# Optimization experiments

Measured on AMD Instinct MI355X. Metric: run time of the kernel, lower is better.

## Reference

```python
import jax, jax.numpy as jnp
import numpy as np

BN_EPS = 1e-5

def _batchnorm(x):
    # BatchNorm1d(affine=False) in training mode: per-feature batch stats, biased var
    m = jnp.mean(x, axis=0)
    v = jnp.var(x, axis=0)
    return (x - m) * jax.lax.rsqrt(v + BN_EPS)

def setup_inputs() -> dict:
    key = jax.random.key(0)
    ks = jax.random.split(key, 8)
    B, S, H, I = 2, 2048, 1024, 4096
    NE, NS, K = 16384, 128, 16
    return {
        "hidden_states": jax.random.normal(ks[0], (B, S, H), dtype=jnp.float32),
        "gate_w": jax.random.normal(ks[1], (I, H), dtype=jnp.float32) * 0.02,
        "up_w": jax.random.normal(ks[2], (I, H), dtype=jnp.float32) * 0.02,
        "down_w": jax.random.normal(ks[3], (H, I), dtype=jnp.float32) * 0.02,
        "router_x_w": jax.random.normal(ks[4], (NS, H), dtype=jnp.float32) * 0.02,
        "router_y_w": jax.random.normal(ks[5], (NS, H), dtype=jnp.float32) * 0.02,
        "up_embed": jax.random.normal(ks[6], (NE, H), dtype=jnp.float32) * 0.02,
        "down_embed": jax.random.normal(ks[7], (NE, H), dtype=jnp.float32) * 0.02,
        "top_k": K,
    }

def reference(hidden_states, gate_w, up_w, down_w, router_x_w, router_y_w, up_embed, down_embed, top_k):
    B, S, H = hidden_states.shape
    ns = router_x_w.shape[0]  # num_expert_sqrt
    x = hidden_states.reshape(-1, H)  # [N, H], N = B*S

    # product-key router: two grid log-softmaxes, outer-sum, global top-k
    lpx = jax.nn.log_softmax(_batchnorm(x @ router_x_w.T), axis=-1)  # [N, ns]
    lpy = jax.nn.log_softmax(_batchnorm(x @ router_y_w.T), axis=-1)  # [N, ns]
    all_scores = (lpx[:, :, None] + lpy[:, None, :]).reshape(-1, ns * ns)  # [N, ns^2]
    scores, indices = jax.lax.top_k(all_scores, top_k)  # [N, k]
    routing_weights = jnp.exp(scores)

    # per-token expert embedding gather + small bmm chain (PEER-style)
    ue = up_embed[indices]    # [N, k, H]
    de = down_embed[indices]  # [N, k, H]
    ew = jnp.einsum('nkh,nh->nk', ue, x)
    ew = jax.nn.silu(ew) * routing_weights
    experts_states = jnp.einsum('nk,nkh->nh', ew, de).reshape(B, S, H)

    # dense gated MLP
    dense = (jax.nn.silu(x @ gate_w.T) * (x @ up_w.T)) @ down_w.T
    return dense.reshape(B, S, H) + experts_states
```

## Files before the change

kernel.cpp:

```cpp
#include <hip/hip_runtime.h>

typedef float f32x4 __attribute__((ext_vector_type(4)));
typedef short bf16x8 __attribute__((ext_vector_type(8)));
typedef unsigned short u16;

#define NEG_INF (-1e30f)

__device__ __forceinline__ u16 f2bf(float f) {
    unsigned u = __builtin_bit_cast(unsigned, f);
    unsigned r = u + 0x7FFFu + ((u >> 16) & 1u);
    return (u16)(r >> 16);
}
__device__ __forceinline__ unsigned pk2(float a, float b) {
    unsigned r;
    asm("v_cvt_pk_bf16_f32 %0, %1, %2" : "=v"(r) : "v"(a), "v"(b));
    return r;
}

__device__ __forceinline__ float wave_max(float v) {
    #pragma unroll
    for (int o = 32; o > 0; o >>= 1) v = fmaxf(v, __shfl_xor(v, o, 64));
    return v;
}
__device__ __forceinline__ float wave_sum(float v) {
    #pragma unroll
    for (int o = 32; o > 0; o >>= 1) v += __shfl_xor(v, o, 64);
    return v;
}
__device__ __forceinline__ void wave_argmax(float& v, int& i) {
    #pragma unroll
    for (int o = 32; o > 0; o >>= 1) {
        float ov = __shfl_xor(v, o, 64);
        int oi = __shfl_xor(i, o, 64);
        if (ov > v || (ov == v && oi < i)) { v = ov; i = oi; }
    }
}

__device__ __forceinline__ void g2l16(const void* g, void* l) {
    __builtin_amdgcn_global_load_lds((__attribute__((address_space(1))) void*)g,
                                     (__attribute__((address_space(3))) void*)l,
                                     16, 0, 0);
}
__device__ __forceinline__ int swz8(int row, int c) { return c ^ (row & 7); }
__device__ __forceinline__ int swz4(int row, int c) { return c ^ ((row >> 1) & 3); }

template<int NTHR>
__device__ __forceinline__ void stageA64(const u16* __restrict__ src, int ld,
                                         u16* dst, int tid) {
    #pragma unroll
    for (int r = 0; r < 2; ++r) {
        int e = r * NTHR * 8 + tid * 8;
        int row = e >> 6, c = (e >> 3) & 7;
        g2l16(src + (size_t)row * ld + swz8(row, c) * 8, dst + e);
    }
}
__device__ __forceinline__ void stageA32(const u16* __restrict__ src, int ld,
                                         u16* dst, int tid) {
    #pragma unroll
    for (int r = 0; r < 2; ++r) {
        int e = r * 2048 + tid * 8;
        int row = e >> 5, c = (e >> 3) & 3;
        g2l16(src + (size_t)row * ld + swz4(row, c) * 8, dst + e);
    }
}

__device__ __forceinline__ void loadT64_256(const float* __restrict__ src, int ld,
                                            int tid, float4* v) {
    int row = tid >> 2, col = (tid & 3) * 16;
    const float* s = src + (size_t)row * ld + col;
    v[0] = *reinterpret_cast<const float4*>(s);
    v[1] = *reinterpret_cast<const float4*>(s + 4);
    v[2] = *reinterpret_cast<const float4*>(s + 8);
    v[3] = *reinterpret_cast<const float4*>(s + 12);
}
__device__ __forceinline__ void writeT64_256(const float4* v, u16* dst, int tid) {
    int row = tid >> 2, c0 = (tid & 3) * 2;
    uint4 p0 = { pk2(v[0].x, v[0].y), pk2(v[0].z, v[0].w), pk2(v[1].x, v[1].y), pk2(v[1].z, v[1].w) };
    uint4 p1 = { pk2(v[2].x, v[2].y), pk2(v[2].z, v[2].w), pk2(v[3].x, v[3].y), pk2(v[3].z, v[3].w) };
    *reinterpret_cast<uint4*>(dst + row * 64 + swz8(row, c0) * 8) = p0;
    *reinterpret_cast<uint4*>(dst + row * 64 + swz8(row, c0 + 1) * 8) = p1;
}
__device__ __forceinline__ void loadT64_512(const float* __restrict__ src, int ld,
                                            int tid, float4* v) {
    int row = tid >> 3, col = (tid & 7) * 8;
    const float* s = src + (size_t)row * ld + col;
    v[0] = *reinterpret_cast<const float4*>(s);
    v[1] = *reinterpret_cast<const float4*>(s + 4);
}
__device__ __forceinline__ void writeT64_512(const float4* v, u16* dst, int tid) {
    int row = tid >> 3, c = tid & 7;
    uint4 p = { pk2(v[0].x, v[0].y), pk2(v[0].z, v[0].w), pk2(v[1].x, v[1].y), pk2(v[1].z, v[1].w) };
    *reinterpret_cast<uint4*>(dst + row * 64 + swz8(row, c) * 8) = p;
}
__device__ __forceinline__ void loadT32(const float* __restrict__ src, int ld,
                                        int tid, float4* v) {
    int row = tid >> 1, col = (tid & 1) * 16;
    const float* s = src + (size_t)row * ld + col;
    v[0] = *reinterpret_cast<const float4*>(s);
    v[1] = *reinterpret_cast<const float4*>(s + 4);
    v[2] = *reinterpret_cast<const float4*>(s + 8);
    v[3] = *reinterpret_cast<const float4*>(s + 12);
}
__device__ __forceinline__ void writeT32(const float4* v, u16* dst, int tid) {
    int row = tid >> 1, c0 = (tid & 1) * 2;
    uint4 p0 = { pk2(v[0].x, v[0].y), pk2(v[0].z, v[0].w), pk2(v[1].x, v[1].y), pk2(v[1].z, v[1].w) };
    uint4 p1 = { pk2(v[2].x, v[2].y), pk2(v[2].z, v[2].w), pk2(v[3].x, v[3].y), pk2(v[3].z, v[3].w) };
    *reinterpret_cast<uint4*>(dst + row * 32 + swz4(row, c0) * 8) = p0;
    *reinterpret_cast<uint4*>(dst + row * 32 + swz4(row, c0 + 1) * 8) = p1;
}

__device__ __forceinline__ bf16x8 frag64s(const u16* lds, int row0, int ks, int lane) {
    int row = row0 + (lane & 15);
    int c = ks * 4 + (lane >> 4);
    return *reinterpret_cast<const bf16x8*>(lds + row * 64 + swz8(row, c) * 8);
}
__device__ __forceinline__ bf16x8 frag32s(const u16* lds, int row0, int lane) {
    int row = row0 + (lane & 15);
    int c = lane >> 4;
    return *reinterpret_cast<const bf16x8*>(lds + row * 32 + swz4(row, c) * 8);
}

__global__ void conv_x(const float* __restrict__ s, u16* __restrict__ d) {
    size_t i = (size_t)blockIdx.x * 256 + threadIdx.x;
    float4 v = *reinterpret_cast<const float4*>(s + i * 4);
    uint2 pk;
    pk.x = pk2(v.x, v.y); pk.y = pk2(v.z, v.w);
    *reinterpret_cast<uint2*>(d + i * 4) = pk;
}

template<bool ABF>
__global__ __launch_bounds__(256, 2) void gemm_router(
    const float* __restrict__ Xf, const u16* __restrict__ Xb,
    const float* __restrict__ RX, const float* __restrict__ RY,
    float* __restrict__ R) {
    __shared__ __align__(16) u16 As[2][4096];
    __shared__ __align__(16) u16 Bs[2][4096];
    int tid = threadIdx.x, lane = tid & 63, wave = tid >> 6;
    int rowBase = blockIdx.y * 64, colBase = blockIdx.x * 64;
    const float* Bp = (blockIdx.x < 2) ? RX + (size_t)colBase * 1024
                                       : RY + (size_t)(colBase - 128) * 1024;
    int wm = (wave >> 1) * 32, wn = (wave & 1) * 32;
    f32x4 acc[2][2] = {};
    float4 av[4], bv[4];
    if constexpr (ABF) stageA64<256>(Xb + (size_t)rowBase * 1024, 1024, As[0], tid);
    else               { loadT64_256(Xf + (size_t)rowBase * 1024, 1024, tid, av);
                         writeT64_256(av, As[0], tid); }
    loadT64_256(Bp, 1024, tid, bv);
    writeT64_256(bv, Bs[0], tid);
    __syncthreads();
    int cur = 0;
    for (int t = 0; t < 16; ++t) {
        if (t < 15) {
            int k0 = (t + 1) * 64;
            if constexpr (ABF) stageA64<256>(Xb + (size_t)rowBase * 1024 + k0, 1024, As[cur ^ 1], tid);
            else               loadT64_256(Xf + (size_t)rowBase * 1024 + k0, 1024, tid, av);
            loadT64_256(Bp + k0, 1024, tid, bv);
        }
        #pragma unroll
        for (int ks = 0; ks < 2; ++ks) {
            bf16x8 af[2], bfr[2];
            #pragma unroll
            for (int i = 0; i < 2; ++i) af[i] = frag64s(As[cur], wm + i * 16, ks, lane);
            #pragma unroll
            for (int j = 0; j < 2; ++j) bfr[j] = frag64s(Bs[cur], wn + j * 16, ks, lane);
            #pragma unroll
            for (int i = 0; i < 2; ++i)
                #pragma unroll
                for (int j = 0; j < 2; ++j)
                    acc[i][j] = __builtin_amdgcn_mfma_f32_16x16x32_bf16(af[i], bfr[j], acc[i][j], 0, 0, 0);
        }
        if (t < 15) {
            if constexpr (!ABF) writeT64_256(av, As[cur ^ 1], tid);
            writeT64_256(bv, Bs[cur ^ 1], tid);
        }
        __syncthreads();
        cur ^= 1;
    }
    int rq = (lane >> 4) * 4, cq = lane & 15;
    #pragma unroll
    for (int i = 0; i < 2; ++i)
        #pragma unroll
        for (int j = 0; j < 2; ++j) {
            int col = colBase + wn + j * 16 + cq;
            #pragma unroll
            for (int r = 0; r < 4; ++r) {
                int row = rowBase + wm + i * 16 + rq + r;
                R[(size_t)row * 256 + col] = acc[i][j][r];
            }
        }
}

template<bool ABF>
__global__ __launch_bounds__(256, 2) void gemm_gateup(
    const float* __restrict__ Xf, const u16* __restrict__ Xb,
    const float* __restrict__ GW, const float* __restrict__ UW,
    u16* __restrict__ H2) {
    __shared__ __align__(16) u16 As[2][4096];
    __shared__ __align__(16) u16 Gs[2][4096];
    __shared__ __align__(16) u16 Us[2][4096];
    int tid = threadIdx.x, lane = tid & 63, wave = tid >> 6;
    int b = blockIdx.x, xcd = b & 7, ii = b >> 3;
    int by = xcd * 4 + (ii >> 5), bx = ii & 31;
    int rowBase = by * 128, colBase = bx * 128;
    const float* Gp = GW + (size_t)colBase * 1024;
    const float* Up = UW + (size_t)colBase * 1024;
    int wm = (wave >> 1) * 64, wn = (wave & 1) * 64;
    f32x4 accg[4][4] = {}, accu[4][4] = {};
    float4 av[4], gv[4], uv[4];
    if constexpr (ABF) stageA32(Xb + (size_t)rowBase * 1024, 1024, As[0], tid);
    else               { loadT32(Xf + (size_t)rowBase * 1024, 1024, tid, av);
                         writeT32(av, As[0], tid); }
    loadT32(Gp, 1024, tid, gv);
    loadT32(Up, 1024, tid, uv);
    writeT32(gv, Gs[0], tid);
    writeT32(uv, Us[0], tid);
    __syncthreads();
    int cur = 0;
    for (int t = 0; t < 32; ++t) {
        if (t < 31) {
            int k0 = (t + 1) * 32;
            if constexpr (ABF) stageA32(Xb + (size_t)rowBase * 1024 + k0, 1024, As[cur ^ 1], tid);
            else               loadT32(Xf + (size_t)rowBase * 1024 + k0, 1024, tid, av);
            loadT32(Gp + k0, 1024, tid, gv);
            loadT32(Up + k0, 1024, tid, uv);
        }
        bf16x8 gf[4], uf[4];
        #pragma unroll
        for (int j = 0; j < 4; ++j) { gf[j] = frag32s(Gs[cur], wn + j * 16, lane);
                                      uf[j] = frag32s(Us[cur], wn + j * 16, lane); }
        #pragma unroll
        for (int i = 0; i < 4; ++i) {
            bf16x8 af = frag32s(As[cur], wm + i * 16, lane);
            #pragma unroll
            for (int j = 0; j < 4; ++j) {
                accg[i][j] = __builtin_amdgcn_mfma_f32_16x16x32_bf16(af, gf[j], accg[i][j], 0, 0, 0);
                accu[i][j] = __builtin_amdgcn_mfma_f32_16x16x32_bf16(af, uf[j], accu[i][j], 0, 0, 0);
            }
        }
        if (t < 31) {
            if constexpr (!ABF) writeT32(av, As[cur ^ 1], tid);
            writeT32(gv, Gs[cur ^ 1], tid);
            writeT32(uv, Us[cur ^ 1], tid);
        }
        __syncthreads();
        cur ^= 1;
    }
    int rq = (lane >> 4) * 4, cq = lane & 15;
    #pragma unroll
    for (int i = 0; i < 4; ++i)
        #pragma unroll
        for (int j = 0; j < 4; ++j) {
            int col = colBase + wn + j * 16 + cq;
            #pragma unroll
            for (int r = 0; r < 4; ++r) {
                int row = rowBase + wm + i * 16 + rq + r;
                float gvv = accg[i][j][r], uvv = accu[i][j][r];
                float h = (gvv / (1.f + __expf(-gvv))) * uvv;
                H2[(size_t)row * 4096 + col] = f2bf(h);
            }
        }
}

__global__ __launch_bounds__(512, 4) void gemm_down_pipe(
    const u16* __restrict__ H2, const float* __restrict__ DW, float* __restrict__ Out) {
    __shared__ __align__(16) u16 As[2][8192];
    __shared__ __align__(16) u16 Bs[2][4096];
    int tid = threadIdx.x, lane = tid & 63, wave = tid >> 6;
    int b = blockIdx.x, xcd = b & 7, ii = b >> 3;
    int by = xcd * 4 + (ii >> 4), bx = ii & 15;
    int rowBase = by * 128, colBase = bx * 64;
    const u16* Ap = H2 + (size_t)rowBase * 4096;
    const float* Bp = DW + (size_t)colBase * 4096;
    int wm = (wave >> 1) * 32, wn = (wave & 1) * 32;
    f32x4 acc[2][2] = {};
    float4 bv[2];
    stageA64<512>(Ap, 4096, As[0], tid);
    loadT64_512(Bp, 4096, tid, bv);
    writeT64_512(bv, Bs[0], tid);
    __syncthreads();
    int cur = 0;
    for (int t = 0; t < 64; ++t) {
        if (t < 63) {
            int k0 = (t + 1) * 64;
            stageA64<512>(Ap + k0, 4096, As[cur ^ 1], tid);
            loadT64_512(Bp + k0, 4096, tid, bv);
        }
        #pragma unroll
        for (int ks = 0; ks < 2; ++ks) {
            bf16x8 af[2], bfr[2];
            #pragma unroll
            for (int i = 0; i < 2; ++i) af[i] = frag64s(As[cur], wm + i * 16, ks, lane);
            #pragma unroll
            for (int j = 0; j < 2; ++j) bfr[j] = frag64s(Bs[cur], wn + j * 16, ks, lane);
            #pragma unroll
            for (int i = 0; i < 2; ++i)
                #pragma unroll
                for (int j = 0; j < 2; ++j)
                    acc[i][j] = __builtin_amdgcn_mfma_f32_16x16x32_bf16(af[i], bfr[j], acc[i][j], 0, 0, 0);
        }
        if (t < 63) writeT64_512(bv, Bs[cur ^ 1], tid);
        __syncthreads();
        cur ^= 1;
    }
    int rq = (lane >> 4) * 4, cq = lane & 15;
    #pragma unroll
    for (int i = 0; i < 2; ++i)
        #pragma unroll
        for (int j = 0; j < 2; ++j) {
            int col = colBase + wn + j * 16 + cq;
            #pragma unroll
            for (int r = 0; r < 4; ++r) {
                int row = rowBase + wm + i * 16 + rq + r;
                size_t o = (size_t)row * 1024 + col;
                Out[o] = acc[i][j][r] + Out[o];
            }
        }
}

__global__ __launch_bounds__(256) void expert_store(
    const float* __restrict__ X, const float* __restrict__ UE, const float* __restrict__ DE,
    const int* __restrict__ idxs, const float* __restrict__ wts, float* __restrict__ Out) {
    int n = blockIdx.x, tid = threadIdx.x;
    int lane = tid & 63, wave = tid >> 6;
    __shared__ float xs[1024];
    __shared__ float ews[16];
    __shared__ int sidx[16];
    __shared__ float swt[16];
    if (tid < 16) {
        sidx[tid] = min(max(idxs[n * 16 + tid], 0), 16383);
        swt[tid] = wts[n * 16 + tid];
    }
    {
        float4 v = reinterpret_cast<const float4*>(X + (size_t)n * 1024)[tid];
        *reinterpret_cast<float4*>(xs + tid * 4) = v;
    }
    __syncthreads();
    #pragma unroll
    for (int q = 0; q < 4; ++q) {
        int e = wave * 4 + q;
        const float* row = UE + (size_t)sidx[e] * 1024;
        float acc = 0.f;
        #pragma unroll
        for (int c = 0; c < 4; ++c) {
            int h = c * 256 + lane * 4;
            float4 a = *reinterpret_cast<const float4*>(row + h);
            float4 xv = *reinterpret_cast<const float4*>(xs + h);
            acc += a.x * xv.x + a.y * xv.y + a.z * xv.z + a.w * xv.w;
        }
        acc = wave_sum(acc);
        if (lane == 0) {
            float s = acc / (1.f + __expf(-acc));
            ews[e] = s * swt[e];
        }
    }
    __syncthreads();
    float4 a = make_float4(0.f, 0.f, 0.f, 0.f);
    int h = tid * 4;
    #pragma unroll
    for (int e = 0; e < 16; ++e) {
        const float* row = DE + (size_t)sidx[e] * 1024;
        float4 v = *reinterpret_cast<const float4*>(row + h);
        float w = ews[e];
        a.x += w * v.x; a.y += w * v.y;
        a.z += w * v.z; a.w += w * v.w;
    }
    reinterpret_cast<float4*>(Out + (size_t)n * 1024)[tid] = a;
}

__global__ void bn_stats(const float* __restrict__ R, float* __restrict__ stats) {
    int c = threadIdx.x;
    int r0 = blockIdx.x * 64;
    float s = 0.f, s2 = 0.f;
    for (int r = r0; r < r0 + 64; ++r) {
        float v = R[(size_t)r * 256 + c];
        s += v; s2 += v * v;
    }
    atomicAdd(&stats[c], s);
    atomicAdd(&stats[256 + c], s2);
}

__global__ __launch_bounds__(64) void router_topk(
    const float* __restrict__ R, const float* __restrict__ stats,
    int* __restrict__ idx_out, float* __restrict__ wt_out) {
    int n = blockIdx.x, lane = threadIdx.x;
    const float invN = 1.0f / 4096.0f;
    float z[4];
    #pragma unroll
    for (int p = 0; p < 4; ++p) {
        int c = p * 64 + lane;
        float mean = stats[c] * invN;
        float var = fmaxf(stats[256 + c] * invN - mean * mean, 0.f);
        float v = R[(size_t)n * 256 + c];
        z[p] = (v - mean) * rsqrtf(var + 1e-5f);
    }
    float mx = wave_max(fmaxf(z[0], z[1]));
    float sx = __logf(wave_sum(__expf(z[0] - mx) + __expf(z[1] - mx)));
    float lx0 = z[0] - mx - sx, lx1 = z[1] - mx - sx;
    float my = wave_max(fmaxf(z[2], z[3]));
    float sy = __logf(wave_sum(__expf(z[2] - my) + __expf(z[3] - my)));
    float ly0 = z[2] - my - sy, ly1 = z[3] - my - sy;

    __shared__ float tx[16], ty[16];
    __shared__ int txc[16], tyc[16];
    float v0 = lx0, v1 = lx1;
    for (int t = 0; t < 16; ++t) {
        float bv; int bc;
        if (v1 > v0) { bv = v1; bc = lane + 64; } else { bv = v0; bc = lane; }
        wave_argmax(bv, bc);
        if (lane == 0) { tx[t] = bv; txc[t] = bc; }
        if (bc == lane) v0 = NEG_INF;
        else if (bc == lane + 64) v1 = NEG_INF;
    }
    v0 = ly0; v1 = ly1;
    for (int t = 0; t < 16; ++t) {
        float bv; int bc;
        if (v1 > v0) { bv = v1; bc = lane + 64; } else { bv = v0; bc = lane; }
        wave_argmax(bv, bc);
        if (lane == 0) { ty[t] = bv; tyc[t] = bc; }
        if (bc == lane) v0 = NEG_INF;
        else if (bc == lane + 64) v1 = NEG_INF;
    }
    __syncthreads();
    float cv[4]; int ci[4];
    #pragma unroll
    for (int p = 0; p < 4; ++p) {
        int pid = p * 64 + lane;
        cv[p] = tx[pid >> 4] + ty[pid & 15];
        ci[p] = pid;
    }
    for (int t = 0; t < 16; ++t) {
        float bv = cv[0]; int bc = ci[0];
        #pragma unroll
        for (int p = 1; p < 4; ++p)
            if (cv[p] > bv) { bv = cv[p]; bc = ci[p]; }
        wave_argmax(bv, bc);
        if (lane == 0) {
            idx_out[n * 16 + t] = txc[bc >> 4] * 128 + tyc[bc & 15];
            wt_out[n * 16 + t] = __expf(bv);
        }
        #pragma unroll
        for (int p = 0; p < 4; ++p)
            if (ci[p] == bc) cv[p] = NEG_INF;
    }
}

extern "C" void kernel_launch(void* const* d_in, const int* in_sizes, int n_in,
                              void* d_out, int out_size, void* d_ws, size_t ws_size,
                              hipStream_t stream) {
    const float* x   = (const float*)d_in[0];
    const float* gw  = (const float*)d_in[1];
    const float* uw  = (const float*)d_in[2];
    const float* dw  = (const float*)d_in[3];
    const float* rxw = (const float*)d_in[4];
    const float* ryw = (const float*)d_in[5];
    const float* ue  = (const float*)d_in[6];
    const float* de  = (const float*)d_in[7];
    float* out = (float*)d_out;

    char* p = (char*)d_ws;
    float* stats = (float*)p; p += 16384;
    int*   idxb  = (int*)p;   p += 262144;
    float* wtb   = (float*)p; p += 262144;
    float* R     = (float*)p;
    u16*   H2    = (u16*)p;

    bool useXb = ws_size >= 42483712ull;
    u16* xb = (u16*)((char*)d_ws + 34095104ull);

    hipMemsetAsync(stats, 0, 512 * sizeof(float), stream);
    if (useXb) conv_x<<<4096, 256, 0, stream>>>(x, xb);

    if (useXb) gemm_router<true ><<<dim3(4, 64), 256, 0, stream>>>(x, xb, rxw, ryw, R);
    else       gemm_router<false><<<dim3(4, 64), 256, 0, stream>>>(x, (const u16*)x, rxw, ryw, R);
    bn_stats<<<64, 256, 0, stream>>>(R, stats);
    router_topk<<<4096, 64, 0, stream>>>(R, stats, idxb, wtb);
    expert_store<<<4096, 256, 0, stream>>>(x, ue, de, idxb, wtb, out);

    if (useXb) gemm_gateup<true ><<<1024, 256, 0, stream>>>(x, xb, gw, uw, H2);
    else       gemm_gateup<false><<<1024, 256, 0, stream>>>(x, (const u16*)x, gw, uw, H2);
    gemm_down_pipe<<<512, 512, 0, stream>>>(H2, dw, out);
}
```

Measured before the change: 515.9 us.

## Pre-convert MLP weights to bf16 once per call and retile down GEMM

Adds a conv_all kernel that converts x and the gate, up and down weights to bf16 in workspace, as long as the workspace is large enough. The gate/up and down GEMMs can then stage bf16 tiles directly instead of loading fp32 and packing in-loop. The down GEMM is also reworked from 512-thread 128-row tiles to 256-thread 64-row tiles with more blocks, and gateup's launch bounds are raised to 3 blocks per SM. The cost is an extra conversion pass over roughly 48MB of weights per call, and the new path only runs if ws_size reaches the larger threshold.

Result: slower. 565.8 us (+9.7%).

```diff
diff --git a/kernel.cpp b/kernel.cpp
--- a/kernel.cpp
+++ b/kernel.cpp
@@ -80,18 +80,6 @@
     *reinterpret_cast<uint4*>(dst + row * 64 + swz8(row, c0) * 8) = p0;
     *reinterpret_cast<uint4*>(dst + row * 64 + swz8(row, c0 + 1) * 8) = p1;
 }
-__device__ __forceinline__ void loadT64_512(const float* __restrict__ src, int ld,
-                                            int tid, float4* v) {
-    int row = tid >> 3, col = (tid & 7) * 8;
-    const float* s = src + (size_t)row * ld + col;
-    v[0] = *reinterpret_cast<const float4*>(s);
-    v[1] = *reinterpret_cast<const float4*>(s + 4);
-}
-__device__ __forceinline__ void writeT64_512(const float4* v, u16* dst, int tid) {
-    int row = tid >> 3, c = tid & 7;
-    uint4 p = { pk2(v[0].x, v[0].y), pk2(v[0].z, v[0].w), pk2(v[1].x, v[1].y), pk2(v[1].z, v[1].w) };
-    *reinterpret_cast<uint4*>(dst + row * 64 + swz8(row, c) * 8) = p;
-}
 __device__ __forceinline__ void loadT32(const float* __restrict__ src, int ld,
                                         int tid, float4* v) {
     int row = tid >> 1, col = (tid & 1) * 16;
@@ -126,6 +114,24 @@
     uint2 pk;
     pk.x = pk2(v.x, v.y); pk.y = pk2(v.z, v.w);
     *reinterpret_cast<uint2*>(d + i * 4) = pk;
+}
+__global__ void conv_all(const float* __restrict__ s0, const float* __restrict__ s1,
+                         const float* __restrict__ s2, const float* __restrict__ s3,
+                         u16* __restrict__ d0, u16* __restrict__ d1,
+                         u16* __restrict__ d2, u16* __restrict__ d3) {
+    int b = blockIdx.x, t = threadIdx.x;
+    int seg = b >> 10;
+    const float* s = seg == 0 ? s0 : seg == 1 ? s1 : seg == 2 ? s2 : s3;
+    u16* d = seg == 0 ? d0 : seg == 1 ? d1 : seg == 2 ? d2 : d3;
+    int base = (b & 1023) * 256 + t;
+    #pragma unroll
+    for (int j = 0; j < 4; ++j) {
+        size_t i = (size_t)base + (size_t)j * 262144;
+        float4 v = *reinterpret_cast<const float4*>(s + i * 4);
+        uint2 pk;
+        pk.x = pk2(v.x, v.y); pk.y = pk2(v.z, v.w);
+        *reinterpret_cast<uint2*>(d + i * 4) = pk;
+    }
 }
 
 template<bool ABF>
@@ -190,10 +196,11 @@
         }
 }
 
-template<bool ABF>
-__global__ __launch_bounds__(256, 2) void gemm_gateup(
+template<int MODE>
+__global__ __launch_bounds__(256, 3) void gemm_gateup(
     const float* __restrict__ Xf, const u16* __restrict__ Xb,
-    const float* __restrict__ GW, const float* __restrict__ UW,
+    const float* __restrict__ GWf, const float* __restrict__ UWf,
+    const u16* __restrict__ GWb, const u16* __restrict__ UWb,
     u16* __restrict__ H2) {
     __shared__ __align__(16) u16 As[2][4096];
     __shared__ __align__(16) u16 Gs[2][4096];
@@ -202,27 +209,35 @@
     int b = blockIdx.x, xcd = b & 7, ii = b >> 3;
     int by = xcd * 4 + (ii >> 5), bx = ii & 31;
     int rowBase = by * 128, colBase = bx * 128;
-    const float* Gp = GW + (size_t)colBase * 1024;
-    const float* Up = UW + (size_t)colBase * 1024;
     int wm = (wave >> 1) * 64, wn = (wave & 1) * 64;
     f32x4 accg[4][4] = {}, accu[4][4] = {};
     float4 av[4], gv[4], uv[4];
-    if constexpr (ABF) stageA32(Xb + (size_t)rowBase * 1024, 1024, As[0], tid);
-    else               { loadT32(Xf + (size_t)rowBase * 1024, 1024, tid, av);
-                         writeT32(av, As[0], tid); }
-    loadT32(Gp, 1024, tid, gv);
-    loadT32(Up, 1024, tid, uv);
-    writeT32(gv, Gs[0], tid);
-    writeT32(uv, Us[0], tid);
+    if constexpr (MODE >= 1) stageA32(Xb + (size_t)rowBase * 1024, 1024, As[0], tid);
+    else                     { loadT32(Xf + (size_t)rowBase * 1024, 1024, tid, av);
+                               writeT32(av, As[0], tid); }
+    if constexpr (MODE == 2) {
+        stageA32(GWb + (size_t)colBase * 1024, 1024, Gs[0], tid);
+        stageA32(UWb + (size_t)colBase * 1024, 1024, Us[0], tid);
+    } else {
+        loadT32(GWf + (size_t)colBase * 1024, 1024, tid, gv);
+        loadT32(UWf + (size_t)colBase * 1024, 1024, tid, uv);
+        writeT32(gv, Gs[0], tid);
+        writeT32(uv, Us[0], tid);
+    }
     __syncthreads();
     int cur = 0;
     for (int t = 0; t < 32; ++t) {
         if (t < 31) {
             int k0 = (t + 1) * 32;
-            if constexpr (ABF) stageA32(Xb + (size_t)rowBase * 1024 + k0, 1024, As[cur ^ 1], tid);
-            else               loadT32(Xf + (size_t)rowBase * 1024 + k0, 1024, tid, av);
-            loadT32(Gp + k0, 1024, tid, gv);
-            loadT32(Up + k0, 1024, tid, uv);
+            if constexpr (MODE >= 1) stageA32(Xb + (size_t)rowBase * 1024 + k0, 1024, As[cur ^ 1], tid);
+            else                     loadT32(Xf + (size_t)rowBase * 1024 + k0, 1024, tid, av);
+            if constexpr (MODE == 2) {
+                stageA32(GWb + (size_t)colBase * 1024 + k0, 1024, Gs[cur ^ 1], tid);
+                stageA32(UWb + (size_t)colBase * 1024 + k0, 1024, Us[cur ^ 1], tid);
+            } else {
+                loadT32(GWf + (size_t)colBase * 1024 + k0, 1024, tid, gv);
+                loadT32(UWf + (size_t)colBase * 1024 + k0, 1024, tid, uv);
+            }
         }
         bf16x8 gf[4], uf[4];
         #pragma unroll
@@ -238,9 +253,9 @@
             }
         }
         if (t < 31) {
-            if constexpr (!ABF) writeT32(av, As[cur ^ 1], tid);
-            writeT32(gv, Gs[cur ^ 1], tid);
-            writeT32(uv, Us[cur ^ 1], tid);
+            if constexpr (MODE == 0) writeT32(av, As[cur ^ 1], tid);
+            if constexpr (MODE < 2) { writeT32(gv, Gs[cur ^ 1], tid);
+                                      writeT32(uv, Us[cur ^ 1], tid); }
         }
         __syncthreads();
         cur ^= 1;
@@ -261,29 +276,32 @@
         }
 }
 
-__global__ __launch_bounds__(512, 4) void gemm_down_pipe(
-    const u16* __restrict__ H2, const float* __restrict__ DW, float* __restrict__ Out) {
-    __shared__ __align__(16) u16 As[2][8192];
+template<bool BW16>
+__global__ __launch_bounds__(256, 4) void gemm_down64(
+    const u16* __restrict__ H2, const float* __restrict__ DWf, const u16* __restrict__ DWb,
+    float* __restrict__ Out) {
+    __shared__ __align__(16) u16 As[2][4096];
     __shared__ __align__(16) u16 Bs[2][4096];
     int tid = threadIdx.x, lane = tid & 63, wave = tid >> 6;
     int b = blockIdx.x, xcd = b & 7, ii = b >> 3;
-    int by = xcd * 4 + (ii >> 4), bx = ii & 15;
-    int rowBase = by * 128, colBase = bx * 64;
+    int by = xcd * 8 + (ii >> 4), bx = ii & 15;
+    int rowBase = by * 64, colBase = bx * 64;
     const u16* Ap = H2 + (size_t)rowBase * 4096;
-    const float* Bp = DW + (size_t)colBase * 4096;
     int wm = (wave >> 1) * 32, wn = (wave & 1) * 32;
     f32x4 acc[2][2] = {};
-    float4 bv[2];
-    stageA64<512>(Ap, 4096, As[0], tid);
-    loadT64_512(Bp, 4096, tid, bv);
-    writeT64_512(bv, Bs[0], tid);
+    float4 bv[4];
+    stageA64<256>(Ap, 4096, As[0], tid);
+    if constexpr (BW16) stageA64<256>(DWb + (size_t)colBase * 4096, 4096, Bs[0], tid);
+    else                { loadT64_256(DWf + (size_t)colBase * 4096, 4096, tid, bv);
+                          writeT64_256(bv, Bs[0], tid); }
     __syncthreads();
     int cur = 0;
     for (int t = 0; t < 64; ++t) {
         if (t < 63) {
             int k0 = (t + 1) * 64;
-            stageA64<512>(Ap + k0, 4096, As[cur ^ 1], tid);
-            loadT64_512(Bp + k0, 4096, tid, bv);
+            stageA64<256>(Ap + k0, 4096, As[cur ^ 1], tid);
+            if constexpr (BW16) stageA64<256>(DWb + (size_t)colBase * 4096 + k0, 4096, Bs[cur ^ 1], tid);
+            else                loadT64_256(DWf + (size_t)colBase * 4096 + k0, 4096, tid, bv);
         }
         #pragma unroll
         for (int ks = 0; ks < 2; ++ks) {
@@ -298,7 +316,7 @@
                 for (int j = 0; j < 2; ++j)
                     acc[i][j] = __builtin_amdgcn_mfma_f32_16x16x32_bf16(af[i], bfr[j], acc[i][j], 0, 0, 0);
         }
-        if (t < 63) writeT64_512(bv, Bs[cur ^ 1], tid);
+        if (t < 63) { if constexpr (!BW16) writeT64_256(bv, Bs[cur ^ 1], tid); }
         __syncthreads();
         cur ^= 1;
     }
@@ -464,19 +482,26 @@
     float* R     = (float*)p;
     u16*   H2    = (u16*)p;
 
-    bool useXb = ws_size >= 42483712ull;
-    u16* xb = (u16*)((char*)d_ws + 34095104ull);
+    u16* xb  = (u16*)((char*)d_ws + 34095104ull);
+    u16* gwb = (u16*)((char*)d_ws + 42483712ull);
+    u16* uwb = (u16*)((char*)d_ws + 50872320ull);
+    u16* dwb = (u16*)((char*)d_ws + 59260928ull);
+    int tier = ws_size >= 67649536ull ? 2 : ws_size >= 42483712ull ? 1 : 0;
 
     hipMemsetAsync(stats, 0, 512 * sizeof(float), stream);
-    if (useXb) conv_x<<<4096, 256, 0, stream>>>(x, xb);
-
-    if (useXb) gemm_router<true ><<<dim3(4, 64), 256, 0, stream>>>(x, xb, rxw, ryw, R);
-    else       gemm_router<false><<<dim3(4, 64), 256, 0, stream>>>(x, (const u16*)x, rxw, ryw, R);
+    if (tier == 2)      conv_all<<<4096, 256, 0, stream>>>(x, gw, uw, dw, xb, gwb, uwb, dwb);
+    else if (tier == 1) conv_x<<<4096, 256, 0, stream>>>(x, xb);
+
+    if (tier >= 1) gemm_router<true ><<<dim3(4, 64), 256, 0, stream>>>(x, xb, rxw, ryw, R);
+    else           gemm_router<false><<<dim3(4, 64), 256, 0, stream>>>(x, (const u16*)x, rxw, ryw, R);
     bn_stats<<<64, 256, 0, stream>>>(R, stats);
     router_topk<<<4096, 64, 0, stream>>>(R, stats, idxb, wtb);
     expert_store<<<4096, 256, 0, stream>>>(x, ue, de, idxb, wtb, out);
 
-    if (useXb) gemm_gateup<true ><<<1024, 256, 0, stream>>>(x, xb, gw, uw, H2);
-    else       gemm_gateup<false><<<1024, 256, 0, stream>>>(x, (const u16*)x, gw, uw, H2);
-    gemm_down_pipe<<<512, 512, 0, stream>>>(H2, dw, out);
-}
+    if (tier == 2)      gemm_gateup<2><<<1024, 256, 0, stream>>>(x, xb, gw, uw, gwb, uwb, H2);
+    else if (tier == 1) gemm_gateup<1><<<1024, 256, 0, stream>>>(x, xb, gw, uw, nullptr, nullptr, H2);
+    else                gemm_gateup<0><<<1024, 256, 0, stream>>>(x, (const u16*)x, gw, uw, nullptr, nullptr, H2);
+
+    if (tier == 2) gemm_down64<true ><<<1024, 256, 0, stream>>>(H2, dw, dwb, out);
+    else           gemm_down64<false><<<1024, 256, 0, stream>>>(H2, dw, (const u16*)dw, out);
+}
```
